# Kernel optimization log

Measured on AMD Instinct MI355X. Metric: run time of the kernel, lower is better.

## Reference

```python
import jax, jax.numpy as jnp
import numpy as np

B, I, J, DIM, H, DH = 2, 2048, 2048, 512, 8, 64
INNER = H * DH  # 512
SCALE = DH ** -0.5


def setup_inputs() -> dict:
    key = jax.random.key(0)
    ks = jax.random.split(key, 10)
    w = lambda k, shp: jax.random.normal(k, shp, dtype=jnp.float32) * 0.02
    return {
        "x": jax.random.normal(ks[0], (B, I, DIM), dtype=jnp.float32),
        "context": jax.random.normal(ks[1], (B, J, DIM), dtype=jnp.float32),
        "w_qk": w(ks[2], (DIM, INNER)),
        "w_cqk": w(ks[3], (DIM, INNER)),
        "w_v": w(ks[4], (DIM, INNER)),
        "w_cv": w(ks[5], (DIM, INNER)),
        "w_out": w(ks[6], (INNER, DIM)),
        "b_out": jnp.zeros((DIM,), dtype=jnp.float32),
        "w_cout": w(ks[7], (INNER, DIM)),
        "b_cout": jnp.zeros((DIM,), dtype=jnp.float32),
    }


def _split_heads(t):
    # [b, n, h*d] -> [b, h, n, d]
    b, n, _ = t.shape
    return t.reshape(b, n, H, DH).transpose(0, 2, 1, 3)


def reference(x, context, w_qk, w_cqk, w_v, w_cv, w_out, b_out, w_cout, b_cout):
    # projections (no bias, matching nn.Linear(..., bias=False))
    qk = _split_heads(x @ w_qk)            # [b,h,i,d]
    cqk = _split_heads(context @ w_cqk)    # [b,h,j,d]
    v = _split_heads(x @ w_v)              # [b,h,i,d]
    cv = _split_heads(context @ w_cv)      # [b,h,j,d]

    sim = jnp.einsum('bhid,bhjd->bhij', qk, cqk) * SCALE  # [b,h,i,j]

    attn = jax.nn.softmax(sim, axis=-1)        # row softmax over j
    context_attn = jax.nn.softmax(sim, axis=-2)  # column softmax over i

    out = jnp.einsum('bhij,bhjd->bhid', attn, cv)           # [b,h,i,d]
    context_out = jnp.einsum('bhji,bhjd->bhid', context_attn, v)  # [b,h,j_out=i? -> per einsum: i indexes last of attn]

    # merge heads: [b,h,n,d] -> [b,n,h*d]
    merge = lambda t: t.transpose(0, 2, 1, 3).reshape(t.shape[0], t.shape[2], INNER)
    out = merge(out) @ w_out + b_out                    # [b,i,dim]
    context_out = merge(context_out) @ w_cout + b_cout  # [b,j,dim]
    return (out, context_out)
```

## Files before the change

kernel.cpp:

```cpp
#include <hip/hip_runtime.h>

#define DEVI __device__ __forceinline__

typedef __attribute__((ext_vector_type(8))) short short8;
typedef __attribute__((ext_vector_type(4))) float f32x4;

struct alignas(8) us4 { unsigned short a, b, c, d; };

DEVI unsigned short f2bf(float f) {
    unsigned int u = __float_as_uint(f);
    u += 0x7fffU + ((u >> 16) & 1U);
    return (unsigned short)(u >> 16);
}

DEVI f32x4 mfma16(short8 a, short8 b, f32x4 c) {
    return __builtin_amdgcn_mfma_f32_16x16x32_bf16(a, b, c, 0, 0, 0);
}

#define GLDS(gp, sp) __builtin_amdgcn_global_load_lds( \
    (const __attribute__((address_space(1))) void*)(gp), \
    (__attribute__((address_space(3))) void*)(sp), 16, 0, 0)

__global__ __launch_bounds__(256) void xcvt_kernel(
    const float* __restrict__ x, const float* __restrict__ ctx,
    short* __restrict__ Xb, short* __restrict__ Cb)
{
    const float* s = blockIdx.z ? ctx : x;
    short* d = blockIdx.z ? Cb : Xb;
    size_t t = (size_t)blockIdx.x * 256 + threadIdx.x;
    float4 v = *(const float4*)(s + t * 4);
    us4 o = { f2bf(v.x), f2bf(v.y), f2bf(v.z), f2bf(v.w) };
    *(us4*)(d + t * 4) = o;
}

__global__ __launch_bounds__(256) void trans_kernel(
    const float* w0, const float* w1, const float* w2, const float* w3,
    const float* w4, const float* w5, short* wT)
{
    const float* srcs[6] = {w0, w1, w2, w3, w4, w5};
    const float* src = srcs[blockIdx.z];
    short* dst = wT + (size_t)blockIdx.z * 512 * 512;
    int k0 = blockIdx.x * 64, n0 = blockIdx.y * 64;
    __shared__ float tile[64][65];
    int t = threadIdx.x;
    int r = t >> 2, c0 = (t & 3) * 16;
#pragma unroll
    for (int ii = 0; ii < 4; ++ii) {
        float4 v = *(const float4*)(src + (size_t)(k0 + r) * 512 + n0 + c0 + ii * 4);
        tile[r][c0 + ii * 4 + 0] = v.x;
        tile[r][c0 + ii * 4 + 1] = v.y;
        tile[r][c0 + ii * 4 + 2] = v.z;
        tile[r][c0 + ii * 4 + 3] = v.w;
    }
    __syncthreads();
#pragma unroll
    for (int ii = 0; ii < 4; ++ii) {
        us4 o;
        o.a = f2bf(tile[c0 + ii * 4 + 0][r]);
        o.b = f2bf(tile[c0 + ii * 4 + 1][r]);
        o.c = f2bf(tile[c0 + ii * 4 + 2][r]);
        o.d = f2bf(tile[c0 + ii * 4 + 3][r]);
        *(us4*)(dst + (size_t)(n0 + r) * 512 + k0 + c0 + ii * 4) = o;
    }
}

__global__ __launch_bounds__(256, 4) void proj_kernel(
    const short* __restrict__ Xb, const short* __restrict__ Cb,
    const short* __restrict__ wT,
    short* __restrict__ QK, short* __restrict__ CQK,
    short* __restrict__ VT, short* __restrict__ CVT)
{
    __shared__ short wst[4096];
    __shared__ float ctile[64][69];
    int p = blockIdx.z;
    const short* src = (p & 1) ? Cb : Xb;
    const short* w = wT + (size_t)p * 262144;
    int wid = threadIdx.x >> 6, lane = threadIdx.x & 63, il = lane & 15, q = lane >> 4;
    int mb = blockIdx.x * 64, nb = blockIdx.y * 64;
    int srow = lane >> 3;
    int scol8 = ((lane & 7) ^ srow) * 8;
    const short* arow = src + (size_t)(mb + wid * 16 + il) * 512;
    f32x4 acc[4] = {};
    for (int ck = 0; ck < 8; ++ck) {
        int k0 = ck * 64;
        __syncthreads();
        GLDS(w + (size_t)(nb + wid * 16 + srow) * 512 + k0 + scol8, wst + wid * 1024);
        GLDS(w + (size_t)(nb + wid * 16 + 8 + srow) * 512 + k0 + scol8, wst + wid * 1024 + 512);
        asm volatile("s_waitcnt vmcnt(0)" ::: "memory");
        __syncthreads();
#pragma unroll
        for (int kk = 0; kk < 2; ++kk) {
            short8 a = *(const short8*)(arow + k0 + kk * 32 + q * 8);
#pragma unroll
            for (int nj = 0; nj < 4; ++nj) {
                short8 b = *(const short8*)(wst + (nj * 16 + il) * 64 + ((((kk << 2) + q) ^ (il & 7)) << 3));
                acc[nj] = mfma16(a, b, acc[nj]);
            }
        }
    }
    __syncthreads();
#pragma unroll
    for (int nj = 0; nj < 4; ++nj)
#pragma unroll
        for (int r = 0; r < 4; ++r)
            ctile[wid * 16 + q * 4 + r][nj * 16 + il] = acc[nj][r];
    __syncthreads();
    int t = threadIdx.x, row = t >> 2, seg = (t & 3) * 16;
    short tmp[16];
    int h = blockIdx.y;
    if (p < 2) {
        short* dst = p ? CQK : QK;
        int i = mb + row, b2 = i >> 11, iL = i & 2047;
#pragma unroll
        for (int e = 0; e < 16; ++e) tmp[e] = (short)f2bf(ctile[row][seg + e]);
        short* dp = dst + (((size_t)b2 * 8 + h) * 2048 + iL) * 64 + seg;
        *(short8*)dp = *(const short8*)tmp;
        *(short8*)(dp + 8) = *(const short8*)(tmp + 8);
    } else {
        short* dst = (p == 2) ? VT : CVT;
        int d = row;
        int i0 = mb + seg, b2 = i0 >> 11, iL = i0 & 2047;
#pragma unroll
        for (int e = 0; e < 16; ++e) tmp[e] = (short)f2bf(ctile[seg + e][d]);
        short* dp = dst + (((size_t)b2 * 8 + h) * 64 + d) * 2048 + iL;
        *(short8*)dp = *(const short8*)tmp;
        *(short8*)(dp + 8) = *(const short8*)(tmp + 8);
    }
}

__global__ __launch_bounds__(512, 4) void attn_kernel(
    const short* __restrict__ QK, const short* __restrict__ CQK,
    const short* __restrict__ VT, const short* __restrict__ CVT,
    short* __restrict__ OUTx, short* __restrict__ OUTc)
{
    __shared__ short At[8192];
    __shared__ short Bt[2][4096];
    __shared__ short Wt[2][4096];
    __shared__ short p_lds[8][16][72];

    int z = blockIdx.z;
    const short* Arows = z ? CQK : QK;
    const short* Bcols = z ? QK : CQK;
    const short* WTm   = z ? VT : CVT;
    short* Om          = z ? OUTc : OUTx;

    int bh = blockIdx.x, ib = blockIdx.y;
    int b_ = bh >> 3, h = bh & 7;
    int w = threadIdx.x >> 6, lane = threadIdx.x & 63, il = lane & 15, q = lane >> 4;
    const short* Ab = Arows + (size_t)bh * 131072;
    const short* Bb = Bcols + (size_t)bh * 131072;
    const short* Wb = WTm + (size_t)bh * 131072;

    int srow = lane >> 3;
    int scol8 = ((lane & 7) ^ srow) * 8;
    int isW = (w >= 4);
    int ws = w & 3;
    int key = (il & 7);

#define STAGE(buf, j0v) do { \
        int r0_ = ws * 16 + srow; \
        if (!isW) { \
            GLDS(Bb + (size_t)((j0v) + r0_) * 64 + scol8, Bt[buf] + ws * 1024); \
            GLDS(Bb + (size_t)((j0v) + r0_ + 8) * 64 + scol8, Bt[buf] + ws * 1024 + 512); \
        } else { \
            GLDS(Wb + (size_t)r0_ * 2048 + (j0v) + scol8, Wt[buf] + ws * 1024); \
            GLDS(Wb + (size_t)(r0_ + 8) * 2048 + (j0v) + scol8, Wt[buf] + ws * 1024 + 512); \
        } } while (0)

    GLDS(Ab + (size_t)(ib * 128 + w * 16 + srow) * 64 + scol8, At + w * 1024);
    GLDS(Ab + (size_t)(ib * 128 + w * 16 + 8 + srow) * 64 + scol8, At + w * 1024 + 512);
    STAGE(0, 0);
    asm volatile("s_waitcnt vmcnt(2)" ::: "memory");

    short8 aq0 = *(const short8*)(At + (w * 16 + il) * 64 + ((q ^ key) << 3));
    short8 aq1 = *(const short8*)(At + (w * 16 + il) * 64 + (((q + 4) ^ key) << 3));

    f32x4 acc[4] = {};
    float s_part[4] = {0.f, 0.f, 0.f, 0.f};
    const float C = 0.18033688011112042f;

    for (int jt = 0; jt < 32; ++jt) {
        int cur = jt & 1;
        if (jt < 31) {
            STAGE(cur ^ 1, (jt + 1) * 64);
            asm volatile("s_waitcnt vmcnt(2)" ::: "memory");
        } else {
            asm volatile("s_waitcnt vmcnt(0)" ::: "memory");
        }
        __builtin_amdgcn_s_barrier();

        f32x4 sim[4];
#pragma unroll
        for (int nj = 0; nj < 4; ++nj) {
            const short* bb = Bt[cur] + (nj * 16 + il) * 64;
            short8 b0 = *(const short8*)(bb + ((q ^ key) << 3));
            short8 b1 = *(const short8*)(bb + (((q + 4) ^ key) << 3));
            f32x4 zz = {};
            zz = mfma16(aq0, b0, zz);
            sim[nj] = mfma16(aq1, b1, zz);
        }
#pragma unroll
        for (int nj = 0; nj < 4; ++nj) {
#pragma unroll
            for (int r = 0; r < 4; ++r) {
                float pv = __builtin_amdgcn_exp2f(sim[nj][r] * C);
                s_part[r] += pv;
                p_lds[w][q * 4 + r][nj * 16 + il] = (short)f2bf(pv);
            }
        }
        short8 pa0 = *(const short8*)(&p_lds[w][il][q * 8]);
        short8 pa1 = *(const short8*)(&p_lds[w][il][32 + q * 8]);
#pragma unroll
        for (int nd = 0; nd < 4; ++nd) {
            const short* vv = Wt[cur] + (nd * 16 + il) * 64;
            short8 v0 = *(const short8*)(vv + ((q ^ key) << 3));
            short8 v1 = *(const short8*)(vv + (((q + 4) ^ key) << 3));
            acc[nd] = mfma16(pa0, v0, acc[nd]);
            acc[nd] = mfma16(pa1, v1, acc[nd]);
        }
        asm volatile("" ::: "memory");
        __builtin_amdgcn_s_barrier();
    }
#undef STAGE

#pragma unroll
    for (int r = 0; r < 4; ++r) {
        float s = s_part[r];
        s += __shfl_xor(s, 1);
        s += __shfl_xor(s, 2);
        s += __shfl_xor(s, 4);
        s += __shfl_xor(s, 8);
        s_part[r] = 1.0f / s;
    }
#pragma unroll
    for (int nd = 0; nd < 4; ++nd) {
        int c = h * 64 + nd * 16 + il;
#pragma unroll
        for (int r = 0; r < 4; ++r) {
            int i = ib * 128 + w * 16 + q * 4 + r;
            Om[((size_t)b_ * 2048 + i) * 512 + c] = (short)f2bf(acc[nd][r] * s_part[r]);
        }
    }
}

__global__ __launch_bounds__(256, 4) void final_kernel(
    const short* __restrict__ OUTx, const short* __restrict__ OUTc,
    const short* __restrict__ wT,
    const float* __restrict__ b_out, const float* __restrict__ b_cout,
    float* __restrict__ dout)
{
    __shared__ short wst[4096];
    int z = blockIdx.z;
    const short* Am = z ? OUTc : OUTx;
    const short* w = wT + (size_t)(4 + z) * 262144;
    const float* bias = z ? b_cout : b_out;
    float* D = dout + (size_t)z * 2097152;
    int wid = threadIdx.x >> 6, lane = threadIdx.x & 63, il = lane & 15, q = lane >> 4;
    int mb = blockIdx.x * 64, nb = blockIdx.y * 64;
    int srow = lane >> 3;
    int scol8 = ((lane & 7) ^ srow) * 8;
    const short* arow = Am + (size_t)(mb + wid * 16 + il) * 512;
    f32x4 acc[4] = {};
    for (int ck = 0; ck < 8; ++ck) {
        int k0 = ck * 64;
        __syncthreads();
        GLDS(w + (size_t)(nb + wid * 16 + srow) * 512 + k0 + scol8, wst + wid * 1024);
        GLDS(w + (size_t)(nb + wid * 16 + 8 + srow) * 512 + k0 + scol8, wst + wid * 1024 + 512);
        asm volatile("s_waitcnt vmcnt(0)" ::: "memory");
        __syncthreads();
#pragma unroll
        for (int kk = 0; kk < 2; ++kk) {
            short8 a = *(const short8*)(arow + k0 + kk * 32 + q * 8);
#pragma unroll
            for (int nj = 0; nj < 4; ++nj) {
                short8 b = *(const short8*)(wst + (nj * 16 + il) * 64 + ((((kk << 2) + q) ^ (il & 7)) << 3));
                acc[nj] = mfma16(a, b, acc[nj]);
            }
        }
    }
#pragma unroll
    for (int nj = 0; nj < 4; ++nj) {
        int c = nb + nj * 16 + il;
        float bi = bias[c];
#pragma unroll
        for (int r = 0; r < 4; ++r) {
            int m = mb + wid * 16 + q * 4 + r;
            D[(size_t)m * 512 + c] = acc[nj][r] + bi;
        }
    }
}

extern "C" void kernel_launch(void* const* d_in, const int* in_sizes, int n_in,
                              void* d_out, int out_size, void* d_ws, size_t ws_size,
                              hipStream_t stream)
{
    (void)in_sizes; (void)n_in; (void)out_size; (void)ws_size;
    const float* x      = (const float*)d_in[0];
    const float* ctx    = (const float*)d_in[1];
    const float* w_qk   = (const float*)d_in[2];
    const float* w_cqk  = (const float*)d_in[3];
    const float* w_v    = (const float*)d_in[4];
    const float* w_cv   = (const float*)d_in[5];
    const float* w_out  = (const float*)d_in[6];
    const float* b_out  = (const float*)d_in[7];
    const float* w_cout = (const float*)d_in[8];
    const float* b_cout = (const float*)d_in[9];
    float* dout = (float*)d_out;

    char* ws = (char*)d_ws;
    const size_t WSZ = (size_t)512 * 512 * 2;
    const size_t TSZ = (size_t)16 * 2048 * 64 * 2;
    short* wT   = (short*)ws;
    short* Xb   = (short*)(ws + 6 * WSZ);
    short* Cb   = (short*)(ws + 6 * WSZ + 1 * TSZ);
    short* QK   = (short*)(ws + 6 * WSZ + 2 * TSZ);
    short* CQK  = (short*)(ws + 6 * WSZ + 3 * TSZ);
    short* VT   = (short*)(ws + 6 * WSZ + 4 * TSZ);
    short* CVT  = (short*)(ws + 6 * WSZ + 5 * TSZ);
    short* OUTx = Xb;
    short* OUTc = Cb;

    xcvt_kernel<<<dim3(2048, 1, 2), 256, 0, stream>>>(x, ctx, Xb, Cb);
    trans_kernel<<<dim3(8, 8, 6), 256, 0, stream>>>(w_qk, w_cqk, w_v, w_cv, w_out, w_cout, wT);
    proj_kernel<<<dim3(64, 8, 4), 256, 0, stream>>>(Xb, Cb, wT, QK, CQK, VT, CVT);
    attn_kernel<<<dim3(16, 16, 2), 512, 0, stream>>>(QK, CQK, VT, CVT, OUTx, OUTc);
    final_kernel<<<dim3(64, 8, 2), 256, 0, stream>>>(OUTx, OUTc, wT, b_out, b_cout, dout);
}
```

Before: 180.1 us.

## Merge prep kernels, double-buffer GEMMs, keep softmax probabilities in registers

Merges the input-convert and weight-transpose kernels into one launch. The projection and final GEMMs now preload the A rows into registers and double-buffer the weight tiles, so only one barrier pair is needed per step. The attention kernel moves to 256 threads, with each wave handling 32 rows. It computes S^T through swapped MFMA operands so the exp'd probabilities can be packed into MFMA A-operands directly, with no LDS round trip. The scale is folded into QK at projection time, and the B-row order is permuted to match the packed layout. This cuts LDS traffic, barriers and launch overhead, at the cost of more register pressure and fragile layout permutations.

```diff
diff --git a/kernel.cpp b/kernel.cpp
--- a/kernel.cpp
+++ b/kernel.cpp
@@ -17,30 +17,42 @@
     return __builtin_amdgcn_mfma_f32_16x16x32_bf16(a, b, c, 0, 0, 0);
 }
 
+DEVI short8 mk8(unsigned a, unsigned b, unsigned c, unsigned d) {
+    union { unsigned u[4]; short8 s; } x;
+    x.u[0] = a; x.u[1] = b; x.u[2] = c; x.u[3] = d;
+    return x.s;
+}
+
 #define GLDS(gp, sp) __builtin_amdgcn_global_load_lds( \
     (const __attribute__((address_space(1))) void*)(gp), \
     (__attribute__((address_space(3))) void*)(sp), 16, 0, 0)
 
-__global__ __launch_bounds__(256) void xcvt_kernel(
+#define VMCNT(n) asm volatile("s_waitcnt vmcnt(" #n ")" ::: "memory")
+
+#define SQC 0.42466089f
+
+__global__ __launch_bounds__(256) void prep_kernel(
     const float* __restrict__ x, const float* __restrict__ ctx,
-    short* __restrict__ Xb, short* __restrict__ Cb)
-{
-    const float* s = blockIdx.z ? ctx : x;
-    short* d = blockIdx.z ? Cb : Xb;
-    size_t t = (size_t)blockIdx.x * 256 + threadIdx.x;
-    float4 v = *(const float4*)(s + t * 4);
-    us4 o = { f2bf(v.x), f2bf(v.y), f2bf(v.z), f2bf(v.w) };
-    *(us4*)(d + t * 4) = o;
-}
-
-__global__ __launch_bounds__(256) void trans_kernel(
     const float* w0, const float* w1, const float* w2, const float* w3,
-    const float* w4, const float* w5, short* wT)
-{
+    const float* w4, const float* w5,
+    short* __restrict__ Xb, short* __restrict__ Cb, short* __restrict__ wT)
+{
+    int z = blockIdx.z;
+    if (z < 2) {
+        const float* s = z ? ctx : x;
+        short* d = z ? Cb : Xb;
+        size_t t = (size_t)blockIdx.x * 256 + threadIdx.x;
+        float4 v = *(const float4*)(s + t * 4);
+        us4 o = { f2bf(v.x), f2bf(v.y), f2bf(v.z), f2bf(v.w) };
+        *(us4*)(d + t * 4) = o;
+        return;
+    }
+    if (blockIdx.x >= 384) return;
     const float* srcs[6] = {w0, w1, w2, w3, w4, w5};
-    const float* src = srcs[blockIdx.z];
-    short* dst = wT + (size_t)blockIdx.z * 512 * 512;
-    int k0 = blockIdx.x * 64, n0 = blockIdx.y * 64;
+    int wz = blockIdx.x >> 6, rem = blockIdx.x & 63;
+    const float* src = srcs[wz];
+    short* dst = wT + (size_t)wz * 262144;
+    int k0 = (rem >> 3) * 64, n0 = (rem & 7) * 64;
     __shared__ float tile[64][65];
     int t = threadIdx.x;
     int r = t >> 2, c0 = (t & 3) * 16;
@@ -70,49 +82,62 @@
     short* __restrict__ QK, short* __restrict__ CQK,
     short* __restrict__ VT, short* __restrict__ CVT)
 {
-    __shared__ short wst[4096];
-    __shared__ float ctile[64][69];
+    __shared__ __align__(16) char smem[17664];
+    short (*wst)[4096] = (short (*)[4096])smem;
+    float (*ctile)[69] = (float (*)[69])smem;
+
     int p = blockIdx.z;
     const short* src = (p & 1) ? Cb : Xb;
-    const short* w = wT + (size_t)p * 262144;
+    const short* wm = wT + (size_t)p * 262144;
     int wid = threadIdx.x >> 6, lane = threadIdx.x & 63, il = lane & 15, q = lane >> 4;
     int mb = blockIdx.x * 64, nb = blockIdx.y * 64;
-    int srow = lane >> 3;
-    int scol8 = ((lane & 7) ^ srow) * 8;
+    int srow = lane >> 3, scol8 = ((lane & 7) ^ srow) << 3;
+    int key = il & 7;
+    const short* wL0 = wm + (size_t)(nb + wid * 16 + srow) * 512 + scol8;
+    const short* wL1 = wL0 + 8 * 512;
+#define PSTAGE(buf, ck) do { \
+    GLDS(wL0 + (ck) * 64, &wst[buf][wid * 1024]); \
+    GLDS(wL1 + (ck) * 64, &wst[buf][wid * 1024 + 512]); } while (0)
+
+    PSTAGE(0, 0);
     const short* arow = src + (size_t)(mb + wid * 16 + il) * 512;
+    short8 a[16];
+#pragma unroll
+    for (int j = 0; j < 16; ++j) a[j] = *(const short8*)(arow + j * 32 + (q << 3));
+
     f32x4 acc[4] = {};
+#pragma unroll
     for (int ck = 0; ck < 8; ++ck) {
-        int k0 = ck * 64;
-        __syncthreads();
-        GLDS(w + (size_t)(nb + wid * 16 + srow) * 512 + k0 + scol8, wst + wid * 1024);
-        GLDS(w + (size_t)(nb + wid * 16 + 8 + srow) * 512 + k0 + scol8, wst + wid * 1024 + 512);
-        asm volatile("s_waitcnt vmcnt(0)" ::: "memory");
-        __syncthreads();
+        int buf = ck & 1;
+        if (ck < 7) { PSTAGE(buf ^ 1, ck + 1); VMCNT(2); } else { VMCNT(0); }
+        __builtin_amdgcn_s_barrier();
 #pragma unroll
         for (int kk = 0; kk < 2; ++kk) {
-            short8 a = *(const short8*)(arow + k0 + kk * 32 + q * 8);
 #pragma unroll
             for (int nj = 0; nj < 4; ++nj) {
-                short8 b = *(const short8*)(wst + (nj * 16 + il) * 64 + ((((kk << 2) + q) ^ (il & 7)) << 3));
-                acc[nj] = mfma16(a, b, acc[nj]);
-            }
-        }
-    }
-    __syncthreads();
+                short8 b = *(const short8*)(&wst[buf][(nj * 16 + il) * 64 + ((((kk << 2) + q) ^ key) << 3)]);
+                acc[nj] = mfma16(a[ck * 2 + kk], b, acc[nj]);
+            }
+        }
+        asm volatile("" ::: "memory");
+        __builtin_amdgcn_s_barrier();
+    }
+#undef PSTAGE
+
 #pragma unroll
     for (int nj = 0; nj < 4; ++nj)
 #pragma unroll
         for (int r = 0; r < 4; ++r)
             ctile[wid * 16 + q * 4 + r][nj * 16 + il] = acc[nj][r];
     __syncthreads();
-    int t = threadIdx.x, row = t >> 2, seg = (t & 3) * 16;
+    int t = threadIdx.x, row = t >> 2, seg = (t & 3) << 4;
     short tmp[16];
     int h = blockIdx.y;
     if (p < 2) {
         short* dst = p ? CQK : QK;
         int i = mb + row, b2 = i >> 11, iL = i & 2047;
 #pragma unroll
-        for (int e = 0; e < 16; ++e) tmp[e] = (short)f2bf(ctile[row][seg + e]);
+        for (int e = 0; e < 16; ++e) tmp[e] = (short)f2bf(ctile[row][seg + e] * SQC);
         short* dp = dst + (((size_t)b2 * 8 + h) * 2048 + iL) * 64 + seg;
         *(short8*)dp = *(const short8*)tmp;
         *(short8*)(dp + 8) = *(const short8*)(tmp + 8);
@@ -128,23 +153,25 @@
     }
 }
 
-__global__ __launch_bounds__(512, 4) void attn_kernel(
+__global__ __launch_bounds__(256, 3) void attn_kernel(
     const short* __restrict__ QK, const short* __restrict__ CQK,
     const short* __restrict__ VT, const short* __restrict__ CVT,
     short* __restrict__ OUTx, short* __restrict__ OUTc)
 {
-    __shared__ short At[8192];
-    __shared__ short Bt[2][4096];
-    __shared__ short Wt[2][4096];
-    __shared__ short p_lds[8][16][72];
-
-    int z = blockIdx.z;
+    __shared__ __align__(16) short At[8192];
+    __shared__ __align__(16) short Bt[2][4096];
+    __shared__ __align__(16) short Wt[2][4096];
+
+    int flat = blockIdx.x + (blockIdx.y << 4) + (blockIdx.z << 8);
+    int bh = flat & 15;
+    int ib = (flat >> 4) & 15;
+    int z = flat >> 8;
+
     const short* Arows = z ? CQK : QK;
     const short* Bcols = z ? QK : CQK;
     const short* WTm   = z ? VT : CVT;
     short* Om          = z ? OUTc : OUTx;
 
-    int bh = blockIdx.x, ib = blockIdx.y;
     int b_ = bh >> 3, h = bh & 7;
     int w = threadIdx.x >> 6, lane = threadIdx.x & 63, il = lane & 15, q = lane >> 4;
     const short* Ab = Arows + (size_t)bh * 131072;
@@ -152,93 +179,116 @@
     const short* Wb = WTm + (size_t)bh * 131072;
 
     int srow = lane >> 3;
-    int scol8 = ((lane & 7) ^ srow) * 8;
-    int isW = (w >= 4);
-    int ws = w & 3;
-    int key = (il & 7);
-
-#define STAGE(buf, j0v) do { \
-        int r0_ = ws * 16 + srow; \
-        if (!isW) { \
-            GLDS(Bb + (size_t)((j0v) + r0_) * 64 + scol8, Bt[buf] + ws * 1024); \
-            GLDS(Bb + (size_t)((j0v) + r0_ + 8) * 64 + scol8, Bt[buf] + ws * 1024 + 512); \
-        } else { \
-            GLDS(Wb + (size_t)r0_ * 2048 + (j0v) + scol8, Wt[buf] + ws * 1024); \
-            GLDS(Wb + (size_t)(r0_ + 8) * 2048 + (j0v) + scol8, Wt[buf] + ws * 1024 + 512); \
-        } } while (0)
-
-    GLDS(Ab + (size_t)(ib * 128 + w * 16 + srow) * 64 + scol8, At + w * 1024);
-    GLDS(Ab + (size_t)(ib * 128 + w * 16 + 8 + srow) * 64 + scol8, At + w * 1024 + 512);
+    int scol8 = ((lane & 7) ^ srow) << 3;
+    int key = il & 7;
+
+    int p0 = w * 16 + srow, p1 = p0 + 8;
+    int j0p = (p0 & 0x23) | ((p0 & 0x0C) << 1) | ((p0 & 0x10) >> 2);
+    int j1p = (p1 & 0x23) | ((p1 & 0x0C) << 1) | ((p1 & 0x10) >> 2);
+    const short* BbL0 = Bb + j0p * 64 + scol8;
+    const short* BbL1 = Bb + j1p * 64 + scol8;
+    const short* WbL0 = Wb + (size_t)p0 * 2048 + scol8;
+    const short* WbL1 = WbL0 + 8 * 2048;
+
+#define STAGE(buf, jt) do { \
+    GLDS(BbL0 + (jt) * 4096, &Bt[buf][w * 1024]); \
+    GLDS(BbL1 + (jt) * 4096, &Bt[buf][w * 1024 + 512]); \
+    GLDS(WbL0 + (jt) * 64, &Wt[buf][w * 1024]); \
+    GLDS(WbL1 + (jt) * 64, &Wt[buf][w * 1024 + 512]); } while (0)
+
+    {
+        const short* AbL = Ab + (size_t)(ib * 128 + w * 32 + srow) * 64 + scol8;
+        GLDS(AbL, &At[w * 2048]);
+        GLDS(AbL + 512, &At[w * 2048 + 512]);
+        GLDS(AbL + 1024, &At[w * 2048 + 1024]);
+        GLDS(AbL + 1536, &At[w * 2048 + 1536]);
+    }
     STAGE(0, 0);
-    asm volatile("s_waitcnt vmcnt(2)" ::: "memory");
-
-    short8 aq0 = *(const short8*)(At + (w * 16 + il) * 64 + ((q ^ key) << 3));
-    short8 aq1 = *(const short8*)(At + (w * 16 + il) * 64 + (((q + 4) ^ key) << 3));
-
-    f32x4 acc[4] = {};
-    float s_part[4] = {0.f, 0.f, 0.f, 0.f};
-    const float C = 0.18033688011112042f;
+    VMCNT(4);
+
+    short8 aq[2][2];
+#pragma unroll
+    for (int rg = 0; rg < 2; ++rg) {
+        const short* base = &At[(w * 32 + rg * 16 + il) * 64];
+        aq[rg][0] = *(const short8*)(base + ((q ^ key) << 3));
+        aq[rg][1] = *(const short8*)(base + (((q + 4) ^ key) << 3));
+    }
+
+    f32x4 acc[2][4] = {};
+    float s_acc[2] = {0.f, 0.f};
 
     for (int jt = 0; jt < 32; ++jt) {
         int cur = jt & 1;
-        if (jt < 31) {
-            STAGE(cur ^ 1, (jt + 1) * 64);
-            asm volatile("s_waitcnt vmcnt(2)" ::: "memory");
-        } else {
-            asm volatile("s_waitcnt vmcnt(0)" ::: "memory");
-        }
-        __builtin_amdgcn_s_barrier();
-
-        f32x4 sim[4];
+        if (jt < 31) { STAGE(cur ^ 1, jt + 1); VMCNT(4); } else { VMCNT(0); }
+        __builtin_amdgcn_s_barrier();
+
+        short8 b0[4], b1[4];
 #pragma unroll
         for (int nj = 0; nj < 4; ++nj) {
-            const short* bb = Bt[cur] + (nj * 16 + il) * 64;
-            short8 b0 = *(const short8*)(bb + ((q ^ key) << 3));
-            short8 b1 = *(const short8*)(bb + (((q + 4) ^ key) << 3));
-            f32x4 zz = {};
-            zz = mfma16(aq0, b0, zz);
-            sim[nj] = mfma16(aq1, b1, zz);
-        }
-#pragma unroll
-        for (int nj = 0; nj < 4; ++nj) {
-#pragma unroll
-            for (int r = 0; r < 4; ++r) {
-                float pv = __builtin_amdgcn_exp2f(sim[nj][r] * C);
-                s_part[r] += pv;
-                p_lds[w][q * 4 + r][nj * 16 + il] = (short)f2bf(pv);
-            }
-        }
-        short8 pa0 = *(const short8*)(&p_lds[w][il][q * 8]);
-        short8 pa1 = *(const short8*)(&p_lds[w][il][32 + q * 8]);
+            const short* bb = &Bt[cur][(nj * 16 + il) * 64];
+            b0[nj] = *(const short8*)(bb + ((q ^ key) << 3));
+            b1[nj] = *(const short8*)(bb + (((q + 4) ^ key) << 3));
+        }
+
+        unsigned pw[2][8];
+#pragma unroll
+        for (int rg = 0; rg < 2; ++rg) {
+#pragma unroll
+            for (int nj = 0; nj < 4; ++nj) {
+                f32x4 zz = {};
+                zz = mfma16(b0[nj], aq[rg][0], zz);
+                zz = mfma16(b1[nj], aq[rg][1], zz);
+                float e0 = __builtin_amdgcn_exp2f(zz[0]);
+                float e1 = __builtin_amdgcn_exp2f(zz[1]);
+                float e2 = __builtin_amdgcn_exp2f(zz[2]);
+                float e3 = __builtin_amdgcn_exp2f(zz[3]);
+                s_acc[rg] += (e0 + e1) + (e2 + e3);
+                pw[rg][nj * 2 + 0] = ((unsigned)f2bf(e1) << 16) | (unsigned)f2bf(e0);
+                pw[rg][nj * 2 + 1] = ((unsigned)f2bf(e3) << 16) | (unsigned)f2bf(e2);
+            }
+        }
+        short8 pa0[2] = { mk8(pw[0][0], pw[0][1], pw[0][2], pw[0][3]),
+                          mk8(pw[1][0], pw[1][1], pw[1][2], pw[1][3]) };
+        short8 pa1[2] = { mk8(pw[0][4], pw[0][5], pw[0][6], pw[0][7]),
+                          mk8(pw[1][4], pw[1][5], pw[1][6], pw[1][7]) };
+
 #pragma unroll
         for (int nd = 0; nd < 4; ++nd) {
-            const short* vv = Wt[cur] + (nd * 16 + il) * 64;
+            const short* vv = &Wt[cur][(nd * 16 + il) * 64];
             short8 v0 = *(const short8*)(vv + ((q ^ key) << 3));
             short8 v1 = *(const short8*)(vv + (((q + 4) ^ key) << 3));
-            acc[nd] = mfma16(pa0, v0, acc[nd]);
-            acc[nd] = mfma16(pa1, v1, acc[nd]);
+#pragma unroll
+            for (int rg = 0; rg < 2; ++rg) {
+                acc[rg][nd] = mfma16(pa0[rg], v0, acc[rg][nd]);
+                acc[rg][nd] = mfma16(pa1[rg], v1, acc[rg][nd]);
+            }
         }
         asm volatile("" ::: "memory");
         __builtin_amdgcn_s_barrier();
     }
 #undef STAGE
 
-#pragma unroll
-    for (int r = 0; r < 4; ++r) {
-        float s = s_part[r];
-        s += __shfl_xor(s, 1);
-        s += __shfl_xor(s, 2);
-        s += __shfl_xor(s, 4);
-        s += __shfl_xor(s, 8);
-        s_part[r] = 1.0f / s;
-    }
-#pragma unroll
-    for (int nd = 0; nd < 4; ++nd) {
-        int c = h * 64 + nd * 16 + il;
-#pragma unroll
-        for (int r = 0; r < 4; ++r) {
-            int i = ib * 128 + w * 16 + q * 4 + r;
-            Om[((size_t)b_ * 2048 + i) * 512 + c] = (short)f2bf(acc[nd][r] * s_part[r]);
+    f32x4 inv[2];
+#pragma unroll
+    for (int rg = 0; rg < 2; ++rg) {
+        float s = s_acc[rg];
+        s += __shfl_xor(s, 16);
+        s += __shfl_xor(s, 32);
+#pragma unroll
+        for (int r = 0; r < 4; ++r)
+            inv[rg][r] = 1.0f / __shfl(s, q * 4 + r);
+    }
+
+#pragma unroll
+    for (int rg = 0; rg < 2; ++rg) {
+#pragma unroll
+        for (int nd = 0; nd < 4; ++nd) {
+#pragma unroll
+            for (int r = 0; r < 4; ++r) {
+                int i = ib * 128 + w * 32 + rg * 16 + q * 4 + r;
+                Om[((size_t)b_ * 2048 + i) * 512 + h * 64 + nd * 16 + il] =
+                    (short)f2bf(acc[rg][nd][r] * inv[rg][r]);
+            }
         }
     }
 }
@@ -249,35 +299,47 @@
     const float* __restrict__ b_out, const float* __restrict__ b_cout,
     float* __restrict__ dout)
 {
-    __shared__ short wst[4096];
+    __shared__ __align__(16) short wst[2][4096];
     int z = blockIdx.z;
     const short* Am = z ? OUTc : OUTx;
-    const short* w = wT + (size_t)(4 + z) * 262144;
+    const short* wm = wT + (size_t)(4 + z) * 262144;
     const float* bias = z ? b_cout : b_out;
     float* D = dout + (size_t)z * 2097152;
     int wid = threadIdx.x >> 6, lane = threadIdx.x & 63, il = lane & 15, q = lane >> 4;
     int mb = blockIdx.x * 64, nb = blockIdx.y * 64;
-    int srow = lane >> 3;
-    int scol8 = ((lane & 7) ^ srow) * 8;
+    int srow = lane >> 3, scol8 = ((lane & 7) ^ srow) << 3;
+    int key = il & 7;
+    const short* wL0 = wm + (size_t)(nb + wid * 16 + srow) * 512 + scol8;
+    const short* wL1 = wL0 + 8 * 512;
+#define FSTAGE(buf, ck) do { \
+    GLDS(wL0 + (ck) * 64, &wst[buf][wid * 1024]); \
+    GLDS(wL1 + (ck) * 64, &wst[buf][wid * 1024 + 512]); } while (0)
+
+    FSTAGE(0, 0);
     const short* arow = Am + (size_t)(mb + wid * 16 + il) * 512;
+    short8 a[16];
+#pragma unroll
+    for (int j = 0; j < 16; ++j) a[j] = *(const short8*)(arow + j * 32 + (q << 3));
+
     f32x4 acc[4] = {};
+#pragma unroll
     for (int ck = 0; ck < 8; ++ck) {
-        int k0 = ck * 64;
-        __syncthreads();
-        GLDS(w + (size_t)(nb + wid * 16 + srow) * 512 + k0 + scol8, wst + wid * 1024);
-        GLDS(w + (size_t)(nb + wid * 16 + 8 + srow) * 512 + k0 + scol8, wst + wid * 1024 + 512);
-        asm volatile("s_waitcnt vmcnt(0)" ::: "memory");
-        __syncthreads();
+        int buf = ck & 1;
+        if (ck < 7) { FSTAGE(buf ^ 1, ck + 1); VMCNT(2); } else { VMCNT(0); }
+        __builtin_amdgcn_s_barrier();
 #pragma unroll
         for (int kk = 0; kk < 2; ++kk) {
-            short8 a = *(const short8*)(arow + k0 + kk * 32 + q * 8);
 #pragma unroll
             for (int nj = 0; nj < 4; ++nj) {
-                short8 b = *(const short8*)(wst + (nj * 16 + il) * 64 + ((((kk << 2) + q) ^ (il & 7)) << 3));
-                acc[nj] = mfma16(a, b, acc[nj]);
-            }
-        }
-    }
+                short8 b = *(const short8*)(&wst[buf][(nj * 16 + il) * 64 + ((((kk << 2) + q) ^ key) << 3)]);
+                acc[nj] = mfma16(a[ck * 2 + kk], b, acc[nj]);
+            }
+        }
+        asm volatile("" ::: "memory");
+        __builtin_amdgcn_s_barrier();
+    }
+#undef FSTAGE
+
 #pragma unroll
     for (int nj = 0; nj < 4; ++nj) {
         int c = nb + nj * 16 + il;
@@ -320,9 +382,9 @@
     short* OUTx = Xb;
     short* OUTc = Cb;
 
-    xcvt_kernel<<<dim3(2048, 1, 2), 256, 0, stream>>>(x, ctx, Xb, Cb);
-    trans_kernel<<<dim3(8, 8, 6), 256, 0, stream>>>(w_qk, w_cqk, w_v, w_cv, w_out, w_cout, wT);
+    prep_kernel<<<dim3(2048, 1, 3), 256, 0, stream>>>(
+        x, ctx, w_qk, w_cqk, w_v, w_cv, w_out, w_cout, Xb, Cb, wT);
     proj_kernel<<<dim3(64, 8, 4), 256, 0, stream>>>(Xb, Cb, wT, QK, CQK, VT, CVT);
-    attn_kernel<<<dim3(16, 16, 2), 512, 0, stream>>>(QK, CQK, VT, CVT, OUTx, OUTc);
+    attn_kernel<<<dim3(16, 16, 2), 256, 0, stream>>>(QK, CQK, VT, CVT, OUTx, OUTc);
     final_kernel<<<dim3(64, 8, 2), 256, 0, stream>>>(OUTx, OUTc, wT, b_out, b_cout, dout);
 }
```

Result: faster. 175.2 us (-2.8%).
